# Kernel tuning notes

Measured on AMD Instinct MI355X. Metric: run time of the kernel, lower is better.

## Reference

```python
import jax, jax.numpy as jnp
import numpy as np

N_EMB = 1024
N_HEAD = 16
EPS = 1e-5


def _linear_params(key, fan_in, fan_out):
    k1, k2 = jax.random.split(key)
    lim = 1.0 / np.sqrt(fan_in)
    W = jax.random.uniform(k1, (fan_in, fan_out), minval=-lim, maxval=lim, dtype=jnp.float32)
    b = jax.random.uniform(k2, (fan_out,), minval=-lim, maxval=lim, dtype=jnp.float32)
    return W, b


def setup_inputs() -> dict:
    key = jax.random.key(0)
    ks = jax.random.split(key, 8)
    x = jax.random.normal(ks[0], (4, 2048, N_EMB), dtype=jnp.float32)
    Wk, bk = _linear_params(ks[1], N_EMB, N_EMB)
    Wq, bq = _linear_params(ks[2], N_EMB, N_EMB)
    Wv, bv = _linear_params(ks[3], N_EMB, N_EMB)
    Wp, bp = _linear_params(ks[4], N_EMB, N_EMB)
    W1, b1 = _linear_params(ks[5], N_EMB, 4 * N_EMB)
    W2, b2 = _linear_params(ks[6], 4 * N_EMB, N_EMB)
    return {
        "x": x,
        "ln1_g": jnp.ones((N_EMB,), jnp.float32), "ln1_b": jnp.zeros((N_EMB,), jnp.float32),
        "Wk": Wk, "bk": bk, "Wq": Wq, "bq": bq, "Wv": Wv, "bv": bv, "Wp": Wp, "bp": bp,
        "ln2_g": jnp.ones((N_EMB,), jnp.float32), "ln2_b": jnp.zeros((N_EMB,), jnp.float32),
        "W1": W1, "b1": b1, "W2": W2, "b2": b2,
        "cond_len": 256,
    }


def _layernorm(x, g, b):
    mu = jnp.mean(x, axis=-1, keepdims=True)
    var = jnp.mean(jnp.square(x - mu), axis=-1, keepdims=True)
    return (x - mu) * jax.lax.rsqrt(var + EPS) * g + b


def _hybrid_mask(T, cond_len):
    # rows attend to all conditioning columns; causal within the remaining block
    i = jnp.arange(T)[:, None]
    j = jnp.arange(T)[None, :]
    return (j < cond_len) | ((i >= cond_len) & (j >= cond_len) & (j <= i))  # [T,T] bool


def _block(x, ln1_g, ln1_b, Wk, bk, Wq, bq, Wv, bv, Wp, bp, ln2_g, ln2_b, W1, b1, W2, b2, cond_len):
    B, T, C = x.shape
    hd = C // N_HEAD
    h = _layernorm(x, ln1_g, ln1_b)
    # QKV: [B,T,C] -> [B,H,T,hd]
    q = (h @ Wq + bq).reshape(B, T, N_HEAD, hd).transpose(0, 2, 1, 3)
    k = (h @ Wk + bk).reshape(B, T, N_HEAD, hd).transpose(0, 2, 1, 3)
    v = (h @ Wv + bv).reshape(B, T, N_HEAD, hd).transpose(0, 2, 1, 3)
    att = jnp.einsum('bhqd,bhkd->bhqk', q, k) * (1.0 / np.sqrt(hd))
    mask = _hybrid_mask(T, cond_len)
    att = jnp.where(mask, att, -jnp.inf)
    att = jax.nn.softmax(att, axis=-1)
    y = jnp.einsum('bhqk,bhkd->bhqd', att, v)
    y = y.transpose(0, 2, 1, 3).reshape(B, T, C)
    x = x + (y @ Wp + bp)
    h2 = _layernorm(x, ln2_g, ln2_b)
    m = jax.nn.gelu(h2 @ W1 + b1, approximate=False) @ W2 + b2
    return x + m


def reference(x, ln1_g, ln1_b, Wk, bk, Wq, bq, Wv, bv, Wp, bp, ln2_g, ln2_b, W1, b1, W2, b2, cond_len):
    return _block(x, ln1_g, ln1_b, Wk, bk, Wq, bq, Wv, bv, Wp, bp, ln2_g, ln2_b, W1, b1, W2, b2, cond_len)
```

## Files before the change

### kernel.cpp

```cpp
#include <hip/hip_runtime.h>

typedef __bf16 bf16;
typedef __attribute__((ext_vector_type(4))) __bf16 bf16x4;
typedef __attribute__((ext_vector_type(8))) __bf16 bf16x8;
typedef __attribute__((ext_vector_type(4))) float f32x4;

__device__ __forceinline__ void stage16(const bf16* g, bf16* l) {
  __builtin_amdgcn_global_load_lds(
      (const __attribute__((address_space(1))) void*)g,
      (__attribute__((address_space(3))) void*)l, 16, 0, 0);
}

__global__ __launch_bounds__(256)
void transpose_f32_bf16(const float* __restrict__ src, bf16* __restrict__ dst, int R, int C)
{
  __shared__ bf16 tile[32][33];
  const int tx = threadIdx.x & 31, ty = threadIdx.x >> 5;
  const int c0 = blockIdx.x * 32, r0 = blockIdx.y * 32;
#pragma unroll
  for (int i = 0; i < 4; ++i)
    tile[ty + i * 8][tx] = (bf16)src[(size_t)(r0 + ty + i * 8) * C + c0 + tx];
  __syncthreads();
#pragma unroll
  for (int i = 0; i < 4; ++i)
    dst[(size_t)(c0 + ty + i * 8) * R + r0 + tx] = tile[tx][ty + i * 8];
}

__global__ __launch_bounds__(256)
void ln_f32_bf16(const float* __restrict__ x, const float* __restrict__ g,
                 const float* __restrict__ bta, bf16* __restrict__ out)
{
  const int row = blockIdx.x * 4 + (threadIdx.x >> 6);
  const int l = threadIdx.x & 63;
  const float* xr = x + (size_t)row * 1024 + l * 16;
  f32x4 a[4];
#pragma unroll
  for (int i = 0; i < 4; ++i) a[i] = ((const f32x4*)xr)[i];
  float s = 0.f, s2 = 0.f;
#pragma unroll
  for (int i = 0; i < 4; ++i)
#pragma unroll
    for (int jj = 0; jj < 4; ++jj) { float vv = a[i][jj]; s += vv; s2 += vv * vv; }
#pragma unroll
  for (int m = 1; m < 64; m <<= 1) { s += __shfl_xor(s, m); s2 += __shfl_xor(s2, m); }
  const float mu = s * (1.0f / 1024.0f);
  const float var = s2 * (1.0f / 1024.0f) - mu * mu;
  const float rs = rsqrtf(var + 1e-5f);
  f32x4 gv[4], bv[4];
#pragma unroll
  for (int i = 0; i < 4; ++i) {
    gv[i] = ((const f32x4*)(g + l * 16))[i];
    bv[i] = ((const f32x4*)(bta + l * 16))[i];
  }
  bf16x8 o0, o1;
#pragma unroll
  for (int i = 0; i < 8; ++i) {
    float v0 = a[i >> 2][i & 3];
    float v1 = a[2 + (i >> 2)][i & 3];
    o0[i] = (bf16)((v0 - mu) * rs * gv[i >> 2][i & 3] + bv[i >> 2][i & 3]);
    o1[i] = (bf16)((v1 - mu) * rs * gv[2 + (i >> 2)][i & 3] + bv[2 + (i >> 2)][i & 3]);
  }
  bf16* orow = out + (size_t)row * 1024 + l * 16;
  ((bf16x8*)orow)[0] = o0;
  ((bf16x8*)orow)[1] = o1;
}

template <int EPI>
__global__ __launch_bounds__(512)
void gemm256b(const bf16* __restrict__ A, const bf16* __restrict__ Bt,
              const float* __restrict__ bias, const float* __restrict__ biasK,
              const float* __restrict__ biasV,
              void* __restrict__ out, void* __restrict__ outK, void* __restrict__ outV,
              int M, int N, int K)
{
  __shared__ bf16 As[2][256 * 32];
  __shared__ bf16 Bs[2][256 * 32];
  const int tid = threadIdx.x;
  const int l = tid & 63;
  const int w = tid >> 6;
  const int wm = w >> 2;
  const int wn = w & 3;
  const int m0 = blockIdx.x * 256;
  const int n0 = blockIdx.y * 256;

  const int srow = tid >> 2;
  const int sG8 = ((tid & 3) ^ ((tid >> 3) & 3)) * 8;
  const bf16* gA = A + (size_t)(m0 + srow) * K + sG8;
  const bf16* gB = Bt + (size_t)(n0 + srow) * K + sG8;
  const int ldsOff = srow * 32 + (tid & 3) * 8;

  const int lrow = l & 15;
  const int rdsl = ((l >> 4) ^ ((lrow >> 1) & 3)) * 8;

  f32x4 acc[8][4] = {};
  const int KT = K >> 5;

#define STAGE(buf, k0)                                                 \
  do {                                                                 \
    stage16(gA + (k0), &As[buf][ldsOff]);                              \
    stage16(gA + (size_t)128 * K + (k0), &As[buf][4096 + ldsOff]);     \
    stage16(gB + (k0), &Bs[buf][ldsOff]);                              \
    stage16(gB + (size_t)128 * K + (k0), &Bs[buf][4096 + ldsOff]);     \
  } while (0)

  STAGE(0, 0);

  for (int kt = 0; kt < KT; ++kt) {
    const int cur = kt & 1;
    __builtin_amdgcn_s_barrier();
    if (kt + 1 < KT) {
      STAGE(cur ^ 1, (kt + 1) << 5);
      asm volatile("s_waitcnt vmcnt(4)" ::: "memory");
    } else {
      asm volatile("s_waitcnt vmcnt(0)" ::: "memory");
    }
    __builtin_amdgcn_sched_barrier(0);
    __builtin_amdgcn_s_barrier();

    bf16x8 a[8], b[4];
#pragma unroll
    for (int mi = 0; mi < 8; ++mi)
      a[mi] = *(const bf16x8*)&As[cur][(wm * 128 + mi * 16 + lrow) * 32 + rdsl];
#pragma unroll
    for (int ni = 0; ni < 4; ++ni)
      b[ni] = *(const bf16x8*)&Bs[cur][(wn * 64 + ni * 16 + lrow) * 32 + rdsl];
    __builtin_amdgcn_s_setprio(1);
#pragma unroll
    for (int mi = 0; mi < 8; ++mi)
#pragma unroll
      for (int ni = 0; ni < 4; ++ni)
        acc[mi][ni] = __builtin_amdgcn_mfma_f32_16x16x32_bf16(a[mi], b[ni], acc[mi][ni], 0, 0, 0);
    __builtin_amdgcn_s_setprio(0);
  }
#undef STAGE

  const int seg = n0 >> 10;
  const float* bp = (EPI == 0) ? (seg == 0 ? bias : (seg == 1 ? biasK : biasV)) : bias;
#pragma unroll
  for (int mi = 0; mi < 8; ++mi) {
#pragma unroll
    for (int ni = 0; ni < 4; ++ni) {
      const int colg = n0 + wn * 64 + ni * 16 + lrow;
      const int col = (EPI == 0) ? (colg & 1023) : colg;
      const float bv = bp[col];
#pragma unroll
      for (int j = 0; j < 4; ++j) {
        const int row = m0 + wm * 128 + mi * 16 + (l >> 4) * 4 + j;
        float val = acc[mi][ni][j] + bv;
        if constexpr (EPI == 0) {
          const int bb = row >> 11, t = row & 2047, hh = col >> 6, d = col & 63;
          if (seg == 0)
            ((bf16*)out)[(((size_t)(bb * 16 + hh) * 2048 + t) * 64) + d] = (bf16)(val * 0.125f);
          else if (seg == 1)
            ((bf16*)outK)[(((size_t)(bb * 16 + hh) * 2048 + t) * 64) + d] = (bf16)val;
          else
            ((bf16*)outV)[(((size_t)(bb * 16 + hh) * 64 + d) * 2048) + t] = (bf16)val;
        } else if constexpr (EPI == 4) {
          const float u = 0.7978845608f * (val + 0.044715f * val * val * val);
          const float e = __expf(2.0f * u);
          const float th = 1.0f - 2.0f / (e + 1.0f);
          ((bf16*)out)[(size_t)row * N + col] = (bf16)(0.5f * val * (1.0f + th));
        }
      }
    }
  }
}

template <int EPI>
__global__ __launch_bounds__(256)
void gemm_bt(const bf16* __restrict__ A, const bf16* __restrict__ Bt,
             const float* __restrict__ bias, void* __restrict__ out,
             const float* __restrict__ res, int M, int N, int K)
{
  __shared__ bf16 As[3][128 * 32];
  __shared__ bf16 Bs[3][128 * 32];
  const int tid = threadIdx.x;
  const int l = tid & 63;
  const int w = tid >> 6;
  const int wm = w >> 1, wn = w & 1;
  const int m0 = blockIdx.x * 128;
  const int n0 = blockIdx.y * 128;

  const int srow = tid >> 2;
  const int sG8 = ((tid & 3) ^ ((tid >> 3) & 3)) * 8;
  const bf16* gA = A + (size_t)(m0 + srow) * K + sG8;
  const bf16* gB = Bt + (size_t)(n0 + srow) * K + sG8;
  const int ldsOff = srow * 32 + (tid & 3) * 8;

  const int lrow = l & 15;
  const int rdsl = ((l >> 4) ^ ((lrow >> 1) & 3)) * 8;

  f32x4 acc[4][4] = {};
  const int KT = K >> 5;

#define STAGE(buf, k0)                                            \
  do {                                                            \
    stage16(gA + (k0), &As[buf][ldsOff]);                         \
    stage16(gA + (size_t)64 * K + (k0), &As[buf][2048 + ldsOff]); \
    stage16(gB + (k0), &Bs[buf][ldsOff]);                         \
    stage16(gB + (size_t)64 * K + (k0), &Bs[buf][2048 + ldsOff]); \
  } while (0)

  STAGE(0, 0);
  if (KT > 1) STAGE(1, 32);

  int cur = 0;
  for (int kt = 0; kt < KT; ++kt) {
    const int stg = (cur == 0) ? 2 : cur - 1;
    __builtin_amdgcn_s_barrier();
    if (kt + 2 < KT) {
      STAGE(stg, (kt + 2) << 5);
      asm volatile("s_waitcnt vmcnt(8)" ::: "memory");
    } else if (kt + 1 < KT) {
      asm volatile("s_waitcnt vmcnt(4)" ::: "memory");
    } else {
      asm volatile("s_waitcnt vmcnt(0)" ::: "memory");
    }
    __builtin_amdgcn_sched_barrier(0);
    __builtin_amdgcn_s_barrier();

    bf16x8 af[4], bfv[4];
#pragma unroll
    for (int i = 0; i < 4; ++i)
      af[i] = *(const bf16x8*)&As[cur][(wm * 64 + i * 16 + lrow) * 32 + rdsl];
#pragma unroll
    for (int i = 0; i < 4; ++i)
      bfv[i] = *(const bf16x8*)&Bs[cur][(wn * 64 + i * 16 + lrow) * 32 + rdsl];
#pragma unroll
    for (int mi = 0; mi < 4; ++mi)
#pragma unroll
      for (int ni = 0; ni < 4; ++ni)
        acc[mi][ni] = __builtin_amdgcn_mfma_f32_16x16x32_bf16(af[mi], bfv[ni], acc[mi][ni], 0, 0, 0);
    cur = (cur == 2) ? 0 : cur + 1;
  }
#undef STAGE

#pragma unroll
  for (int mi = 0; mi < 4; ++mi) {
#pragma unroll
    for (int ni = 0; ni < 4; ++ni) {
      const int col = n0 + wn * 64 + ni * 16 + lrow;
      const float bv = bias[col];
#pragma unroll
      for (int j = 0; j < 4; ++j) {
        const int row = m0 + wm * 64 + mi * 16 + (l >> 4) * 4 + j;
        float val = acc[mi][ni][j] + bv;
        if constexpr (EPI == 3 || EPI == 5) {
          ((float*)out)[(size_t)row * 1024 + col] = val + res[(size_t)row * 1024 + col];
        }
      }
    }
  }
}

__global__ __launch_bounds__(512)
void attn_kernel(const bf16* __restrict__ q, const bf16* __restrict__ k,
                 const bf16* __restrict__ v, bf16* __restrict__ y,
                 const int* __restrict__ condp)
{
  __shared__ bf16 Ks[2][64 * 72];
  __shared__ bf16 Vs[2][64 * 72];
  __shared__ char PsB[8][2048];
  const int tid = threadIdx.x, l = tid & 63, w = tid >> 6;
  const int bx = blockIdx.x;
  const int qt = 15 - (bx >> 6);
  const int bh = bx & 63;
  const int bb = bh >> 4, hh = bh & 15;
  const int cond = condp[0];
  const int iLo = qt * 128;
  const size_t base = (size_t)bh * 2048 * 64;

  const int lrow = l & 15;
  const int g = l >> 4;
  const int lslot = g * 8;

  const int qrow = iLo + w * 16 + lrow;
  const bf16x8 bq0 = *(const bf16x8*)(q + base + (size_t)qrow * 64 + lslot);
  const bf16x8 bq1 = *(const bf16x8*)(q + base + (size_t)qrow * 64 + 32 + lslot);

  f32x4 o[4] = {};
  float m = -1e30f, lsum = 0.f;

  const int ckt = (cond + 63) >> 6;
  int nkt = ((iLo + 127) >> 6) + 1;
  if (nkt < ckt) nkt = ckt;
  const int wHi = iLo + w * 16 + 15;

  const int kr = tid >> 3;
  const int ks8 = (tid & 7) * 8;
  const bf16* kp = k + base + (size_t)kr * 64 + ks8;
  const bf16* vp = v + base + (size_t)kr * 2048 + ks8;

  bf16x8 rk = *(const bf16x8*)kp;
  bf16x8 rv = *(const bf16x8*)vp;
  *(bf16x8*)&Ks[0][kr * 72 + ks8] = rk;
  *(bf16x8*)&Vs[0][kr * 72 + ks8] = rv;
  __syncthreads();

  char* psw = PsB[w];

  for (int kt = 0; kt < nkt; ++kt) {
    const int cur = kt & 1;
    const int j0 = kt << 6;
    const bool pf = (kt + 1 < nkt);
    if (pf) {
      rk = *(const bf16x8*)(kp + (size_t)(j0 + 64) * 64);
      rv = *(const bf16x8*)(vp + j0 + 64);
    }

    const bool active = (j0 < cond) || (j0 <= wHi);
    if (active) {
      f32x4 sfr[4];
      __builtin_amdgcn_s_setprio(1);
#pragma unroll
      for (int nf = 0; nf < 4; ++nf) {
        f32x4 s = {};
        bf16x8 ka0 = *(const bf16x8*)&Ks[cur][(nf * 16 + lrow) * 72 + lslot];
        bf16x8 ka1 = *(const bf16x8*)&Ks[cur][(nf * 16 + lrow) * 72 + 32 + lslot];
        s = __builtin_amdgcn_mfma_f32_16x16x32_bf16(ka0, bq0, s, 0, 0, 0);
        s = __builtin_amdgcn_mfma_f32_16x16x32_bf16(ka1, bq1, s, 0, 0, 0);
        sfr[nf] = s;
      }
      __builtin_amdgcn_s_setprio(0);

      const bool safe = (j0 + 63 < cond) || (j0 + 63 <= iLo + w * 16);
      if (!safe) {
#pragma unroll
        for (int nf = 0; nf < 4; ++nf)
#pragma unroll
          for (int j = 0; j < 4; ++j) {
            const int kc = j0 + nf * 16 + g * 4 + j;
            const bool ok = (kc < cond) || (kc <= qrow);
            sfr[nf][j] = ok ? sfr[nf][j] : -1e30f;
          }
      }

      float pmax = sfr[0][0];
#pragma unroll
      for (int nf = 0; nf < 4; ++nf)
#pragma unroll
        for (int j = 0; j < 4; ++j) pmax = fmaxf(pmax, sfr[nf][j]);
      pmax = fmaxf(pmax, __shfl_xor(pmax, 16));
      pmax = fmaxf(pmax, __shfl_xor(pmax, 32));

      const bool resc = !__all(pmax - m <= 8.0f);
      if (resc) {
        const float mnew = fmaxf(m, pmax);
        const float alpha = __expf(m - mnew);
        m = mnew;
        lsum *= alpha;
        float ar[4];
#pragma unroll
        for (int j = 0; j < 4; ++j) ar[j] = __shfl(alpha, (l & 48) | (g * 4 + j));
#pragma unroll
        for (int df = 0; df < 4; ++df)
#pragma unroll
          for (int j = 0; j < 4; ++j) o[df][j] *= ar[j];
      }

      float rsum = 0.f;
#pragma unroll
      for (int nf = 0; nf < 4; ++nf) {
        bf16x4 pk;
#pragma unroll
        for (int j = 0; j < 4; ++j) {
          const float p = __expf(sfr[nf][j] - m);
          rsum += p;
          pk[j] = (bf16)p;
        }
        const int slot = 2 * nf + (g >> 1);
        const int boff = lrow * 128 + ((slot ^ (lrow & 7)) << 4) + (g & 1) * 8;
        *(bf16x4*)(psw + boff) = pk;
      }
      rsum += __shfl_xor(rsum, 16);
      rsum += __shfl_xor(rsum, 32);
      lsum += rsum;

      const int r0b = lrow * 128 + (((g) ^ (lrow & 7)) << 4);
      const int r1b = lrow * 128 + (((g + 4) ^ (lrow & 7)) << 4);
      const bf16x8 pa0 = *(const bf16x8*)(psw + r0b);
      const bf16x8 pa1 = *(const bf16x8*)(psw + r1b);
      __builtin_amdgcn_s_setprio(1);
#pragma unroll
      for (int df = 0; df < 4; ++df) {
        bf16x8 v0 = *(const bf16x8*)&Vs[cur][(df * 16 + lrow) * 72 + lslot];
        bf16x8 v1 = *(const bf16x8*)&Vs[cur][(df * 16 + lrow) * 72 + 32 + lslot];
        o[df] = __builtin_amdgcn_mfma_f32_16x16x32_bf16(pa0, v0, o[df], 0, 0, 0);
        o[df] = __builtin_amdgcn_mfma_f32_16x16x32_bf16(pa1, v1, o[df], 0, 0, 0);
      }
      __builtin_amdgcn_s_setprio(0);
    }

    if (pf) {
      *(bf16x8*)&Ks[cur ^ 1][kr * 72 + ks8] = rk;
      *(bf16x8*)&Vs[cur ^ 1][kr * 72 + ks8] = rv;
    }
    __syncthreads();
  }

  float lr[4];
#pragma unroll
  for (int j = 0; j < 4; ++j) lr[j] = 1.0f / __shfl(lsum, (l & 48) | (g * 4 + j));
#pragma unroll
  for (int df = 0; df < 4; ++df)
#pragma unroll
    for (int j = 0; j < 4; ++j) {
      const int irow = iLo + w * 16 + g * 4 + j;
      y[((size_t)bb * 2048 + irow) * 1024 + hh * 64 + df * 16 + lrow] = (bf16)(o[df][j] * lr[j]);
    }
}

extern "C" void kernel_launch(void* const* d_in, const int* in_sizes, int n_in,
                              void* d_out, int out_size, void* d_ws, size_t ws_size,
                              hipStream_t stream) {
  const float* x    = (const float*)d_in[0];
  const float* ln1g = (const float*)d_in[1];
  const float* ln1b = (const float*)d_in[2];
  const float* Wk   = (const float*)d_in[3];
  const float* bk   = (const float*)d_in[4];
  const float* Wq   = (const float*)d_in[5];
  const float* bq   = (const float*)d_in[6];
  const float* Wv   = (const float*)d_in[7];
  const float* bv   = (const float*)d_in[8];
  const float* Wp   = (const float*)d_in[9];
  const float* bpb  = (const float*)d_in[10];
  const float* ln2g = (const float*)d_in[11];
  const float* ln2b = (const float*)d_in[12];
  const float* W1   = (const float*)d_in[13];
  const float* b1   = (const float*)d_in[14];
  const float* W2   = (const float*)d_in[15];
  const float* b2   = (const float*)d_in[16];
  const int*  cond  = (const int*)d_in[17];
  float* out = (float*)d_out;

  char* ws = (char*)d_ws;
  const size_t MB = 1024ull * 1024ull;
  if (ws_size < 136 * MB) return;

  bf16*  WqkvT = (bf16*)(ws + 0 * MB);
  bf16*  WpT   = (bf16*)(ws + 6 * MB);
  bf16*  W1T   = (bf16*)(ws + 8 * MB);
  bf16*  W2T   = (bf16*)(ws + 16 * MB);
  float* x2    = (float*)(ws + 24 * MB);
  bf16*  hbuf  = (bf16*)(ws + 56 * MB);
  bf16*  qb    = (bf16*)(ws + 72 * MB);
  bf16*  kb    = (bf16*)(ws + 88 * MB);
  bf16*  vb    = (bf16*)(ws + 104 * MB);
  bf16*  yb    = (bf16*)(ws + 120 * MB);
  bf16*  m1    = (bf16*)(ws + 72 * MB);

  dim3 blk(256);
  transpose_f32_bf16<<<dim3(32, 32), blk, 0, stream>>>(Wq, WqkvT,                1024, 1024);
  transpose_f32_bf16<<<dim3(32, 32), blk, 0, stream>>>(Wk, WqkvT + 1024 * 1024,  1024, 1024);
  transpose_f32_bf16<<<dim3(32, 32), blk, 0, stream>>>(Wv, WqkvT + 2048 * 1024,  1024, 1024);
  transpose_f32_bf16<<<dim3(32, 32), blk, 0, stream>>>(Wp, WpT, 1024, 1024);
  transpose_f32_bf16<<<dim3(128, 32), blk, 0, stream>>>(W1, W1T, 1024, 4096);
  transpose_f32_bf16<<<dim3(32, 128), blk, 0, stream>>>(W2, W2T, 4096, 1024);

  ln_f32_bf16<<<2048, blk, 0, stream>>>(x, ln1g, ln1b, hbuf);

  gemm256b<0><<<dim3(32, 12), dim3(512), 0, stream>>>(hbuf, WqkvT, bq, bk, bv,
                                                      qb, kb, vb, 8192, 3072, 1024);

  attn_kernel<<<dim3(1024), dim3(512), 0, stream>>>(qb, kb, vb, yb, cond);

  gemm_bt<3><<<dim3(64, 8), blk, 0, stream>>>(yb, WpT, bpb, x2, x, 8192, 1024, 1024);
  ln_f32_bf16<<<2048, blk, 0, stream>>>(x2, ln2g, ln2b, hbuf);
  gemm256b<4><<<dim3(32, 16), dim3(512), 0, stream>>>(hbuf, W1T, b1, nullptr, nullptr,
                                                      m1, nullptr, nullptr, 8192, 4096, 1024);
  gemm_bt<5><<<dim3(64, 8), blk, 0, stream>>>(m1, W2T, b2, out, x2, 8192, 1024, 4096);
}
```

Before: 440.4 us.

## Shrink big GEMM tile to 256x128, simplify pipelines, fuse weight transposes

Replaces the six weight-transpose launches with one combined kernel that dispatches tiles by block index. The 256x256 GEMM used for QKV and MLP-up becomes 256x128 with a 4x2 wave layout, launching twice as many blocks with a smaller per-wave accumulator. Both GEMM kernels drop their hand-tuned vmcnt waits, setprio and triple buffering in favour of plain double buffering with __syncthreads. This cuts register and LDS pressure and launch overhead, but lowers operand reuse per block and may hide memory latency less well.

```diff
diff --git a/kernel.cpp b/kernel.cpp
--- a/kernel.cpp
+++ b/kernel.cpp
@@ -11,12 +11,12 @@
       (__attribute__((address_space(3))) void*)l, 16, 0, 0);
 }
 
-__global__ __launch_bounds__(256)
-void transpose_f32_bf16(const float* __restrict__ src, bf16* __restrict__ dst, int R, int C)
+__device__ __forceinline__ void tr_tile(const float* __restrict__ src, bf16* __restrict__ dst,
+                                        int R, int C, int cx, int ry)
 {
   __shared__ bf16 tile[32][33];
   const int tx = threadIdx.x & 31, ty = threadIdx.x >> 5;
-  const int c0 = blockIdx.x * 32, r0 = blockIdx.y * 32;
+  const int c0 = cx * 32, r0 = ry * 32;
 #pragma unroll
   for (int i = 0; i < 4; ++i)
     tile[ty + i * 8][tx] = (bf16)src[(size_t)(r0 + ty + i * 8) * C + c0 + tx];
@@ -24,6 +24,28 @@
 #pragma unroll
   for (int i = 0; i < 4; ++i)
     dst[(size_t)(c0 + ty + i * 8) * R + r0 + tx] = tile[tx][ty + i * 8];
+}
+
+__global__ __launch_bounds__(256)
+void transpose_all(const float* __restrict__ Wq, const float* __restrict__ Wk,
+                   const float* __restrict__ Wv, const float* __restrict__ Wp,
+                   const float* __restrict__ W1, const float* __restrict__ W2,
+                   bf16* __restrict__ WqkvT, bf16* __restrict__ WpT,
+                   bf16* __restrict__ W1T, bf16* __restrict__ W2T)
+{
+  const int id = blockIdx.x;
+  if (id < 4096) {
+    const int seg = id >> 10, t = id & 1023;
+    const float* src = (seg == 0) ? Wq : (seg == 1) ? Wk : (seg == 2) ? Wv : Wp;
+    bf16* dst = (seg == 3) ? WpT : (WqkvT + (size_t)seg * 1024 * 1024);
+    tr_tile(src, dst, 1024, 1024, t & 31, t >> 5);
+  } else if (id < 8192) {
+    const int t = id - 4096;
+    tr_tile(W1, W1T, 1024, 4096, t & 127, t >> 7);
+  } else {
+    const int t = id - 8192;
+    tr_tile(W2, W2T, 4096, 1024, t & 31, t >> 5);
+  }
 }
 
 __global__ __launch_bounds__(256)
@@ -67,21 +89,21 @@
 
 template <int EPI>
 __global__ __launch_bounds__(512)
-void gemm256b(const bf16* __restrict__ A, const bf16* __restrict__ Bt,
-              const float* __restrict__ bias, const float* __restrict__ biasK,
-              const float* __restrict__ biasV,
-              void* __restrict__ out, void* __restrict__ outK, void* __restrict__ outV,
-              int M, int N, int K)
+void gemm_bt256(const bf16* __restrict__ A, const bf16* __restrict__ Bt,
+                const float* __restrict__ bias, const float* __restrict__ biasK,
+                const float* __restrict__ biasV,
+                void* __restrict__ out, void* __restrict__ outK, void* __restrict__ outV,
+                int M, int N, int K)
 {
   __shared__ bf16 As[2][256 * 32];
-  __shared__ bf16 Bs[2][256 * 32];
+  __shared__ bf16 Bs[2][128 * 32];
   const int tid = threadIdx.x;
   const int l = tid & 63;
   const int w = tid >> 6;
-  const int wm = w >> 2;
-  const int wn = w & 3;
+  const int wm = w >> 1;
+  const int wn = w & 1;
   const int m0 = blockIdx.x * 256;
-  const int n0 = blockIdx.y * 256;
+  const int n0 = blockIdx.y * 128;
 
   const int srow = tid >> 2;
   const int sG8 = ((tid & 3) ^ ((tid >> 3) & 3)) * 8;
@@ -92,52 +114,42 @@
   const int lrow = l & 15;
   const int rdsl = ((l >> 4) ^ ((lrow >> 1) & 3)) * 8;
 
-  f32x4 acc[8][4] = {};
+  f32x4 acc[4][4] = {};
   const int KT = K >> 5;
 
-#define STAGE(buf, k0)                                                 \
-  do {                                                                 \
-    stage16(gA + (k0), &As[buf][ldsOff]);                              \
-    stage16(gA + (size_t)128 * K + (k0), &As[buf][4096 + ldsOff]);     \
-    stage16(gB + (k0), &Bs[buf][ldsOff]);                              \
-    stage16(gB + (size_t)128 * K + (k0), &Bs[buf][4096 + ldsOff]);     \
+#define STAGE(buf, k0)                                              \
+  do {                                                              \
+    stage16(gA + (k0), &As[buf][ldsOff]);                           \
+    stage16(gA + (size_t)128 * K + (k0), &As[buf][4096 + ldsOff]);  \
+    stage16(gB + (k0), &Bs[buf][ldsOff]);                           \
   } while (0)
 
   STAGE(0, 0);
 
   for (int kt = 0; kt < KT; ++kt) {
     const int cur = kt & 1;
-    __builtin_amdgcn_s_barrier();
-    if (kt + 1 < KT) {
-      STAGE(cur ^ 1, (kt + 1) << 5);
-      asm volatile("s_waitcnt vmcnt(4)" ::: "memory");
-    } else {
-      asm volatile("s_waitcnt vmcnt(0)" ::: "memory");
-    }
-    __builtin_amdgcn_sched_barrier(0);
-    __builtin_amdgcn_s_barrier();
-
-    bf16x8 a[8], b[4];
-#pragma unroll
-    for (int mi = 0; mi < 8; ++mi)
-      a[mi] = *(const bf16x8*)&As[cur][(wm * 128 + mi * 16 + lrow) * 32 + rdsl];
-#pragma unroll
-    for (int ni = 0; ni < 4; ++ni)
-      b[ni] = *(const bf16x8*)&Bs[cur][(wn * 64 + ni * 16 + lrow) * 32 + rdsl];
-    __builtin_amdgcn_s_setprio(1);
-#pragma unroll
-    for (int mi = 0; mi < 8; ++mi)
+    __syncthreads();
+    if (kt + 1 < KT) STAGE(cur ^ 1, (kt + 1) << 5);
+
+    bf16x8 af[4], bfv[4];
+#pragma unroll
+    for (int i = 0; i < 4; ++i)
+      af[i] = *(const bf16x8*)&As[cur][(wm * 64 + i * 16 + lrow) * 32 + rdsl];
+#pragma unroll
+    for (int i = 0; i < 4; ++i)
+      bfv[i] = *(const bf16x8*)&Bs[cur][(wn * 64 + i * 16 + lrow) * 32 + rdsl];
+#pragma unroll
+    for (int mi = 0; mi < 4; ++mi)
 #pragma unroll
       for (int ni = 0; ni < 4; ++ni)
-        acc[mi][ni] = __builtin_amdgcn_mfma_f32_16x16x32_bf16(a[mi], b[ni], acc[mi][ni], 0, 0, 0);
-    __builtin_amdgcn_s_setprio(0);
+        acc[mi][ni] = __builtin_amdgcn_mfma_f32_16x16x32_bf16(af[mi], bfv[ni], acc[mi][ni], 0, 0, 0);
   }
 #undef STAGE
 
   const int seg = n0 >> 10;
   const float* bp = (EPI == 0) ? (seg == 0 ? bias : (seg == 1 ? biasK : biasV)) : bias;
 #pragma unroll
-  for (int mi = 0; mi < 8; ++mi) {
+  for (int mi = 0; mi < 4; ++mi) {
 #pragma unroll
     for (int ni = 0; ni < 4; ++ni) {
       const int colg = n0 + wn * 64 + ni * 16 + lrow;
@@ -145,7 +157,7 @@
       const float bv = bp[col];
 #pragma unroll
       for (int j = 0; j < 4; ++j) {
-        const int row = m0 + wm * 128 + mi * 16 + (l >> 4) * 4 + j;
+        const int row = m0 + wm * 64 + mi * 16 + (l >> 4) * 4 + j;
         float val = acc[mi][ni][j] + bv;
         if constexpr (EPI == 0) {
           const int bb = row >> 11, t = row & 2047, hh = col >> 6, d = col & 63;
@@ -172,8 +184,8 @@
              const float* __restrict__ bias, void* __restrict__ out,
              const float* __restrict__ res, int M, int N, int K)
 {
-  __shared__ bf16 As[3][128 * 32];
-  __shared__ bf16 Bs[3][128 * 32];
+  __shared__ bf16 As[2][128 * 32];
+  __shared__ bf16 Bs[2][128 * 32];
   const int tid = threadIdx.x;
   const int l = tid & 63;
   const int w = tid >> 6;
@@ -202,22 +214,11 @@
   } while (0)
 
   STAGE(0, 0);
-  if (KT > 1) STAGE(1, 32);
-
-  int cur = 0;
+
   for (int kt = 0; kt < KT; ++kt) {
-    const int stg = (cur == 0) ? 2 : cur - 1;
-    __builtin_amdgcn_s_barrier();
-    if (kt + 2 < KT) {
-      STAGE(stg, (kt + 2) << 5);
-      asm volatile("s_waitcnt vmcnt(8)" ::: "memory");
-    } else if (kt + 1 < KT) {
-      asm volatile("s_waitcnt vmcnt(4)" ::: "memory");
-    } else {
-      asm volatile("s_waitcnt vmcnt(0)" ::: "memory");
-    }
-    __builtin_amdgcn_sched_barrier(0);
-    __builtin_amdgcn_s_barrier();
+    const int cur = kt & 1;
+    __syncthreads();
+    if (kt + 1 < KT) STAGE(cur ^ 1, (kt + 1) << 5);
 
     bf16x8 af[4], bfv[4];
 #pragma unroll
@@ -231,7 +232,6 @@
 #pragma unroll
       for (int ni = 0; ni < 4; ++ni)
         acc[mi][ni] = __builtin_amdgcn_mfma_f32_16x16x32_bf16(af[mi], bfv[ni], acc[mi][ni], 0, 0, 0);
-    cur = (cur == 2) ? 0 : cur + 1;
   }
 #undef STAGE
 
@@ -450,23 +450,19 @@
   bf16*  m1    = (bf16*)(ws + 72 * MB);
 
   dim3 blk(256);
-  transpose_f32_bf16<<<dim3(32, 32), blk, 0, stream>>>(Wq, WqkvT,                1024, 1024);
-  transpose_f32_bf16<<<dim3(32, 32), blk, 0, stream>>>(Wk, WqkvT + 1024 * 1024,  1024, 1024);
-  transpose_f32_bf16<<<dim3(32, 32), blk, 0, stream>>>(Wv, WqkvT + 2048 * 1024,  1024, 1024);
-  transpose_f32_bf16<<<dim3(32, 32), blk, 0, stream>>>(Wp, WpT, 1024, 1024);
-  transpose_f32_bf16<<<dim3(128, 32), blk, 0, stream>>>(W1, W1T, 1024, 4096);
-  transpose_f32_bf16<<<dim3(32, 128), blk, 0, stream>>>(W2, W2T, 4096, 1024);
+  transpose_all<<<dim3(12288), blk, 0, stream>>>(Wq, Wk, Wv, Wp, W1, W2,
+                                                 WqkvT, WpT, W1T, W2T);
 
   ln_f32_bf16<<<2048, blk, 0, stream>>>(x, ln1g, ln1b, hbuf);
 
-  gemm256b<0><<<dim3(32, 12), dim3(512), 0, stream>>>(hbuf, WqkvT, bq, bk, bv,
-                                                      qb, kb, vb, 8192, 3072, 1024);
+  gemm_bt256<0><<<dim3(32, 24), dim3(512), 0, stream>>>(hbuf, WqkvT, bq, bk, bv,
+                                                        qb, kb, vb, 8192, 3072, 1024);
 
   attn_kernel<<<dim3(1024), dim3(512), 0, stream>>>(qb, kb, vb, yb, cond);
 
   gemm_bt<3><<<dim3(64, 8), blk, 0, stream>>>(yb, WpT, bpb, x2, x, 8192, 1024, 1024);
   ln_f32_bf16<<<2048, blk, 0, stream>>>(x2, ln2g, ln2b, hbuf);
-  gemm256b<4><<<dim3(32, 16), dim3(512), 0, stream>>>(hbuf, W1T, b1, nullptr, nullptr,
-                                                      m1, nullptr, nullptr, 8192, 4096, 1024);
+  gemm_bt256<4><<<dim3(32, 32), dim3(512), 0, stream>>>(hbuf, W1T, b1, nullptr, nullptr,
+                                                        m1, nullptr, nullptr, 8192, 4096, 1024);
   gemm_bt<5><<<dim3(64, 8), blk, 0, stream>>>(m1, W2T, b2, out, x2, 8192, 1024, 4096);
 }
```

Result: faster. 388.8 us (median of 2 runs) (-11.7%).
